# Kernel optimization log

Measured on AMD Instinct MI355X. Metric: run time of the kernel, lower is better.

The kernel has to match this reference:

```python
import jax, jax.numpy as jnp
import numpy as np

NEG_SLOPE = 0.2  # LeakyReLU slope from the module


def setup_inputs() -> dict:
    key = jax.random.key(0)
    k1, k2, k3, k4 = jax.random.split(key, 4)
    B, N, C, H, D = 8, 1024, 256, 4, 64
    x = jax.random.normal(k1, (B, N, C), dtype=jnp.float32)
    adj = (jax.random.uniform(k2, (B, N, N)) < 0.05).astype(jnp.float32)
    # nn.Linear weight, stored as (in, out) for x @ W
    W = jax.random.normal(k3, (C, H * D), dtype=jnp.float32) / np.sqrt(C)
    a = jax.random.normal(k4, (1, H, 2 * D), dtype=jnp.float32) * 0.1
    return {"x": x, "adj": adj, "W": W, "a": a}


def reference(x, adj, W, a):
    # x: (B,N,C), adj: (B,N,N), W: (C,H*D), a: (1,H,2D)
    B, N, _ = x.shape
    H = a.shape[1]
    D = a.shape[2] // 2
    Wx = (x @ W).reshape(B, N, H, D)  # (B,N,H,D)
    # (cat([Wx_i, Wx_j]) * a).sum(-1) decomposes into two rank-1 terms:
    a_i, a_j = a[0, :, :D], a[0, :, D:]
    e_i = jnp.einsum('bnhd,hd->bnh', Wx, a_i)  # contribution of target node i
    e_j = jnp.einsum('bjhd,hd->bjh', Wx, a_j)  # contribution of source node j
    e = e_i[:, :, None, :] + e_j[:, None, :, :]  # (B,N,N,H)
    e = jnp.where(e > 0, e, NEG_SLOPE * e)  # LeakyReLU(0.2)
    # add self-loops, mask non-edges with -inf
    adj_self = adj + jnp.eye(N, dtype=adj.dtype)[None]
    mask = (adj_self == 0)[..., None]  # (B,N,N,1)
    e = jnp.where(mask, -jnp.inf, e)
    alpha = jax.nn.softmax(e, axis=2)  # softmax over neighbors j
    # dropout is identity in eval mode
    # torch: einsum('bnjh,bnjhd', alpha, Wx_j) with Wx_j broadcast over n
    out = jnp.einsum('bnjh,bjhd->bnhd', alpha, Wx)
    return out.reshape(B, N, H * D)
```

## Files before the change

### kernel.cpp

```cpp
#include <hip/hip_runtime.h>

#define Nn 1024
#define Cc 256
#define Hh 4
#define Dd 64
#define HD 256
#define LOG2E 1.4426950408889634f
#define WSTRIDE 264

typedef unsigned short u16;
typedef unsigned int u32;
typedef unsigned long long u64;
typedef unsigned char u8;
typedef __bf16 bf16x2 __attribute__((ext_vector_type(2)));
typedef __bf16 bf16x8 __attribute__((ext_vector_type(8)));
typedef float f32x4 __attribute__((ext_vector_type(4)));
typedef u16 u16x8 __attribute__((ext_vector_type(8)));
typedef u32 u32x4 __attribute__((ext_vector_type(4)));

__device__ __forceinline__ float bf2f(u16 v) {
    return __builtin_bit_cast(float, (u32)v << 16);
}
__device__ __forceinline__ u16 f2bf(float f) {
    u32 u = __builtin_bit_cast(u32, f);
    return (u16)((u + 0x7fffu + ((u >> 16) & 1u)) >> 16);
}
__device__ __forceinline__ u32 pk_bf16(float a, float b) {
#if __has_builtin(__builtin_amdgcn_cvt_pk_bf16_f32)
    bf16x2 v = __builtin_amdgcn_cvt_pk_bf16_f32(a, b);
    return __builtin_bit_cast(u32, v);
#else
    return (u32)f2bf(a) | ((u32)f2bf(b) << 16);
#endif
}
__device__ __forceinline__ float fast_exp2(float x) {
#if __has_builtin(__builtin_amdgcn_exp2f)
    return __builtin_amdgcn_exp2f(x);
#else
    float r; asm("v_exp_f32 %0, %1" : "=v"(r) : "v"(x)); return r;
#endif
}

__global__ __launch_bounds__(256) void k_fused(const float* __restrict__ adj,
        u8* __restrict__ bm, const float* __restrict__ x,
        const float* __restrict__ W, const float* __restrict__ a,
        u16* __restrict__ WxTt, float* __restrict__ ei, float* __restrict__ ej) {
    __shared__ u16 ldsw[Dd * WSTRIDE];

    if (blockIdx.x >= 512) {
        int idx = (blockIdx.x - 512) * 256 + threadIdx.x;
        int bn = idx >> 7;
        int byteidx = idx & 127;
        int n = bn & 1023;
        const float* p = adj + ((size_t)bn << 10) + (byteidx << 3);
        float4 v0 = *reinterpret_cast<const float4*>(p);
        float4 v1 = *reinterpret_cast<const float4*>(p + 4);
        u32 bits = 0;
        bits |= (__builtin_bit_cast(u32, v0.x) != 0u) ? 1u : 0u;
        bits |= (__builtin_bit_cast(u32, v0.y) != 0u) ? 2u : 0u;
        bits |= (__builtin_bit_cast(u32, v0.z) != 0u) ? 4u : 0u;
        bits |= (__builtin_bit_cast(u32, v0.w) != 0u) ? 8u : 0u;
        bits |= (__builtin_bit_cast(u32, v1.x) != 0u) ? 16u : 0u;
        bits |= (__builtin_bit_cast(u32, v1.y) != 0u) ? 32u : 0u;
        bits |= (__builtin_bit_cast(u32, v1.z) != 0u) ? 64u : 0u;
        bits |= (__builtin_bit_cast(u32, v1.w) != 0u) ? 128u : 0u;
        if ((n >> 3) == byteidx) bits |= 1u << (n & 7);
        bm[idx] = (u8)bits;
        return;
    }

    int h = blockIdx.x & 3;
    int group = blockIdx.x >> 2;
    int tid = threadIdx.x;

    {
        const float* wrow = W + tid * HD + h * 64;
        #pragma unroll
        for (int c = 0; c < 64; c += 4) {
            float4 wv = *reinterpret_cast<const float4*>(wrow + c);
            u32 p01 = pk_bf16(wv.x, wv.y);
            u32 p23 = pk_bf16(wv.z, wv.w);
            ldsw[(c + 0) * WSTRIDE + tid] = (u16)p01;
            ldsw[(c + 1) * WSTRIDE + tid] = (u16)(p01 >> 16);
            ldsw[(c + 2) * WSTRIDE + tid] = (u16)p23;
            ldsw[(c + 3) * WSTRIDE + tid] = (u16)(p23 >> 16);
        }
    }
    __syncthreads();

    int w = tid >> 6, lane = tid & 63;
    int row_tile = group * 4 + w;
    int m0 = row_tile * 16;
    int b = m0 >> 10;
    int nloc0 = m0 & 1023;
    int c15 = lane & 15;
    int quad = lane >> 4;

    f32x4 acc[4] = {};
    const float* xrow = x + (size_t)(m0 + c15) * Cc + quad * 8;
    #pragma unroll
    for (int k0 = 0; k0 < Cc; k0 += 32) {
        float4 xv0 = *reinterpret_cast<const float4*>(xrow + k0);
        float4 xv1 = *reinterpret_cast<const float4*>(xrow + k0 + 4);
        u32 h0 = pk_bf16(xv0.x, xv0.y);
        u32 h1 = pk_bf16(xv0.z, xv0.w);
        u32 h2 = pk_bf16(xv1.x, xv1.y);
        u32 h3 = pk_bf16(xv1.z, xv1.w);
        u32 l0 = pk_bf16(xv0.x - __builtin_bit_cast(float, h0 << 16),
                         xv0.y - __builtin_bit_cast(float, h0 & 0xffff0000u));
        u32 l1 = pk_bf16(xv0.z - __builtin_bit_cast(float, h1 << 16),
                         xv0.w - __builtin_bit_cast(float, h1 & 0xffff0000u));
        u32 l2 = pk_bf16(xv1.x - __builtin_bit_cast(float, h2 << 16),
                         xv1.y - __builtin_bit_cast(float, h2 & 0xffff0000u));
        u32 l3 = pk_bf16(xv1.z - __builtin_bit_cast(float, h3 << 16),
                         xv1.w - __builtin_bit_cast(float, h3 & 0xffff0000u));
        u32x4 hp = {h0, h1, h2, h3};
        u32x4 lp = {l0, l1, l2, l3};
        bf16x8 ah = __builtin_bit_cast(bf16x8, hp);
        bf16x8 al = __builtin_bit_cast(bf16x8, lp);
        const u16* ldsk = ldsw + k0 + quad * 8;
        #pragma unroll
        for (int t = 0; t < 4; ++t) {
            bf16x8 bh = *reinterpret_cast<const bf16x8*>(ldsk + (t * 16 + c15) * WSTRIDE);
            acc[t] = __builtin_amdgcn_mfma_f32_16x16x32_bf16(ah, bh, acc[t], 0, 0, 0);
            acc[t] = __builtin_amdgcn_mfma_f32_16x16x32_bf16(al, bh, acc[t], 0, 0, 0);
        }
    }
    int bh = b * Hh + h;
    int n_base = nloc0 + quad * 4;
    int chunk = nloc0 >> 5;
    int jq = ((n_base >> 3) & 3);
    int ii = n_base & 7;
    size_t tb = (size_t)bh * 65536 + chunk * 2048 + jq * 128 + c15 * 8 + ii;
    #pragma unroll
    for (int t = 0; t < 4; ++t) {
        uint2 pk2;
        pk2.x = pk_bf16(acc[t][0], acc[t][1]);
        pk2.y = pk_bf16(acc[t][2], acc[t][3]);
        *reinterpret_cast<uint2*>(WxTt + tb + t * 512) = pk2;
    }
    float ai[4], aj[4];
    #pragma unroll
    for (int t = 0; t < 4; ++t) {
        ai[t] = a[h * 2 * Dd + t * 16 + c15];
        aj[t] = a[h * 2 * Dd + Dd + t * 16 + c15];
    }
    #pragma unroll
    for (int r = 0; r < 4; ++r) {
        float si = acc[0][r] * ai[0] + acc[1][r] * ai[1] + acc[2][r] * ai[2] + acc[3][r] * ai[3];
        float sj = acc[0][r] * aj[0] + acc[1][r] * aj[1] + acc[2][r] * aj[2] + acc[3][r] * aj[3];
        #pragma unroll
        for (int off = 1; off < 16; off <<= 1) {
            si += __shfl_xor(si, off);
            sj += __shfl_xor(sj, off);
        }
        if (c15 == 0) {
            int n = nloc0 + quad * 4 + r;
            ei[(size_t)bh * Nn + n] = si * LOG2E;
            ej[(size_t)bh * Nn + n] = sj * LOG2E;
        }
    }
}

__global__ __launch_bounds__(256) void k_attn(const u8* __restrict__ bm,
        const u16* __restrict__ WxTt, const float* __restrict__ eis,
        const float* __restrict__ ejs, float* __restrict__ out) {
    int widx = threadIdx.x >> 6;
    int lane = threadIdx.x & 63;
    int bh = blockIdx.x >> 5;
    int tile = blockIdx.x & 31;
    int b = bh >> 2, h = bh & 3;
    int n0 = tile * 32;
    int col = lane & 15;
    int quad = lane >> 4;

    int r0 = n0 + col, r1 = n0 + 16 + col;
    float ei0 = eis[(size_t)bh * Nn + r0];
    float ei1 = eis[(size_t)bh * Nn + r1];
    const u8* mb0 = bm + ((size_t)(b * Nn + r0)) * 128;
    const u8* mb1 = bm + ((size_t)(b * Nn + r1)) * 128;
    const float* ejrow = ejs + (size_t)bh * Nn + quad * 8;
    const u16* wxplane = WxTt + (size_t)bh * 65536 + lane * 8;

    u16 ov = (col == 0) ? (u16)0x3f80 : (u16)0;
    u16x8 onesu = {ov, ov, ov, ov, ov, ov, ov, ov};
    bf16x8 onesf = __builtin_bit_cast(bf16x8, onesu);

    f32x4 acc0[4] = {}, acc1[4] = {};
    f32x4 accl0 = {}, accl1 = {};
    int jbase = widx * 256;
    #pragma unroll 2
    for (int s = 0; s < 8; ++s) {
        int j0 = jbase + s * 32;
        u32 mw0 = *reinterpret_cast<const u32*>(mb0 + (j0 >> 3));
        u32 mw1 = *reinterpret_cast<const u32*>(mb1 + (j0 >> 3));
        u32 q0 = (mw0 >> (quad * 8)) & 0xffu;
        u32 q1 = (mw1 >> (quad * 8)) & 0xffu;
        float4 eA = *reinterpret_cast<const float4*>(ejrow + j0);
        float4 eB = *reinterpret_cast<const float4*>(ejrow + j0 + 4);
        float ejv[8] = {eA.x, eA.y, eA.z, eA.w, eB.x, eB.y, eB.z, eB.w};
        u32 p0[4], p1[4];
        #pragma unroll
        for (int pi = 0; pi < 4; ++pi) {
            float e_lo = ejv[2 * pi], e_hi = ejv[2 * pi + 1];
            float sa = ei0 + e_lo, sb = ei0 + e_hi;
            sa = fmaxf(sa, 0.2f * sa); sb = fmaxf(sb, 0.2f * sb);
            u32 m0 = (((q0 >> (2 * pi)) & 1u) ? 0xffffu : 0u)
                   | (((q0 >> (2 * pi + 1)) & 1u) ? 0xffff0000u : 0u);
            p0[pi] = pk_bf16(fast_exp2(sa), fast_exp2(sb)) & m0;
            float sc = ei1 + e_lo, sd = ei1 + e_hi;
            sc = fmaxf(sc, 0.2f * sc); sd = fmaxf(sd, 0.2f * sd);
            u32 m1 = (((q1 >> (2 * pi)) & 1u) ? 0xffffu : 0u)
                   | (((q1 >> (2 * pi + 1)) & 1u) ? 0xffff0000u : 0u);
            p1[pi] = pk_bf16(fast_exp2(sc), fast_exp2(sd)) & m1;
        }
        u32x4 pv0 = {p0[0], p0[1], p0[2], p0[3]};
        u32x4 pv1 = {p1[0], p1[1], p1[2], p1[3]};
        bf16x8 a0 = __builtin_bit_cast(bf16x8, pv0);
        bf16x8 a1 = __builtin_bit_cast(bf16x8, pv1);
        const u16* bbase = wxplane + (j0 >> 5) * 2048;
        #pragma unroll
        for (int t = 0; t < 4; ++t) {
            bf16x8 bfr = *reinterpret_cast<const bf16x8*>(bbase + t * 512);
            acc0[t] = __builtin_amdgcn_mfma_f32_16x16x32_bf16(a0, bfr, acc0[t], 0, 0, 0);
            acc1[t] = __builtin_amdgcn_mfma_f32_16x16x32_bf16(a1, bfr, acc1[t], 0, 0, 0);
        }
        accl0 = __builtin_amdgcn_mfma_f32_16x16x32_bf16(a0, onesf, accl0, 0, 0, 0);
        accl1 = __builtin_amdgcn_mfma_f32_16x16x32_bf16(a1, onesf, accl1, 0, 0, 0);
    }

    __shared__ f32x4 lacc[4][8][64];
    __shared__ float lsums[4][2][16];
    #pragma unroll
    for (int t = 0; t < 4; ++t) {
        lacc[widx][t][lane] = acc0[t];
        lacc[widx][4 + t][lane] = acc1[t];
    }
    if (col == 0) {
        #pragma unroll
        for (int r = 0; r < 4; ++r) {
            lsums[widx][0][quad * 4 + r] = accl0[r];
            lsums[widx][1][quad * 4 + r] = accl1[r];
        }
    }
    __syncthreads();
    #pragma unroll
    for (int pp = 0; pp < 2; ++pp) {
        int p = widx * 2 + pp;
        int f = p >> 2, t = p & 3;
        f32x4 v = lacc[0][p][lane];
        v += lacc[1][p][lane];
        v += lacc[2][p][lane];
        v += lacc[3][p][lane];
        #pragma unroll
        for (int r = 0; r < 4; ++r) {
            int rloc = quad * 4 + r;
            float lv = lsums[0][f][rloc] + lsums[1][f][rloc]
                     + lsums[2][f][rloc] + lsums[3][f][rloc];
            int nr = n0 + f * 16 + rloc;
            out[(size_t)(b * Nn + nr) * HD + h * Dd + t * 16 + col] = v[r] * (1.0f / lv);
        }
    }
}

extern "C" void kernel_launch(void* const* d_in, const int* in_sizes, int n_in,
                              void* d_out, int out_size, void* d_ws, size_t ws_size,
                              hipStream_t stream) {
    const float* x   = (const float*)d_in[0];
    const float* adj = (const float*)d_in[1];
    const float* W   = (const float*)d_in[2];
    const float* a   = (const float*)d_in[3];
    float* out = (float*)d_out;

    char* ws = (char*)d_ws;
    u16*   WxTt = (u16*)(ws);
    float* ei   = (float*)(ws + (4u << 20));
    float* ej   = (float*)(ws + (4u << 20) + (128u << 10));
    u8*    bm   = (u8*)(ws + (4u << 20) + (256u << 10));

    k_fused<<<4608, 256, 0, stream>>>(adj, bm, x, W, a, WxTt, ei, ej);
    k_attn<<<1024, 256, 0, stream>>>(bm, WxTt, ei, ej, out);
}
```

Measured before the change: 111.8 us.

## Fuse adjacency bitmask packing into attention kernel and split work across heads

After: 139.2 us. 24.5% more time.

```diff
diff --git a/kernel.cpp b/kernel.cpp
--- a/kernel.cpp
+++ b/kernel.cpp
@@ -10,7 +10,6 @@
 
 typedef unsigned short u16;
 typedef unsigned int u32;
-typedef unsigned long long u64;
 typedef unsigned char u8;
 typedef __bf16 bf16x2 __attribute__((ext_vector_type(2)));
 typedef __bf16 bf16x8 __attribute__((ext_vector_type(8)));
@@ -41,33 +40,10 @@
 #endif
 }
 
-__global__ __launch_bounds__(256) void k_fused(const float* __restrict__ adj,
-        u8* __restrict__ bm, const float* __restrict__ x,
+__global__ __launch_bounds__(256) void k_gemm(const float* __restrict__ x,
         const float* __restrict__ W, const float* __restrict__ a,
         u16* __restrict__ WxTt, float* __restrict__ ei, float* __restrict__ ej) {
     __shared__ u16 ldsw[Dd * WSTRIDE];
-
-    if (blockIdx.x >= 512) {
-        int idx = (blockIdx.x - 512) * 256 + threadIdx.x;
-        int bn = idx >> 7;
-        int byteidx = idx & 127;
-        int n = bn & 1023;
-        const float* p = adj + ((size_t)bn << 10) + (byteidx << 3);
-        float4 v0 = *reinterpret_cast<const float4*>(p);
-        float4 v1 = *reinterpret_cast<const float4*>(p + 4);
-        u32 bits = 0;
-        bits |= (__builtin_bit_cast(u32, v0.x) != 0u) ? 1u : 0u;
-        bits |= (__builtin_bit_cast(u32, v0.y) != 0u) ? 2u : 0u;
-        bits |= (__builtin_bit_cast(u32, v0.z) != 0u) ? 4u : 0u;
-        bits |= (__builtin_bit_cast(u32, v0.w) != 0u) ? 8u : 0u;
-        bits |= (__builtin_bit_cast(u32, v1.x) != 0u) ? 16u : 0u;
-        bits |= (__builtin_bit_cast(u32, v1.y) != 0u) ? 32u : 0u;
-        bits |= (__builtin_bit_cast(u32, v1.z) != 0u) ? 64u : 0u;
-        bits |= (__builtin_bit_cast(u32, v1.w) != 0u) ? 128u : 0u;
-        if ((n >> 3) == byteidx) bits |= 1u << (n & 7);
-        bm[idx] = (u8)bits;
-        return;
-    }
 
     int h = blockIdx.x & 3;
     int group = blockIdx.x >> 2;
@@ -162,103 +138,98 @@
     }
 }
 
-__global__ __launch_bounds__(256) void k_attn(const u8* __restrict__ bm,
+__global__ __launch_bounds__(512) void k_attn(const float* __restrict__ adj,
         const u16* __restrict__ WxTt, const float* __restrict__ eis,
         const float* __restrict__ ejs, float* __restrict__ out) {
-    int widx = threadIdx.x >> 6;
-    int lane = threadIdx.x & 63;
-    int bh = blockIdx.x >> 5;
+    __shared__ u32 maskLds[32][33];
+
+    int tid = threadIdx.x;
+    int b = blockIdx.x >> 5;
     int tile = blockIdx.x & 31;
-    int b = bh >> 2, h = bh & 3;
     int n0 = tile * 32;
+
+    {
+        int row = tid >> 4;
+        int w0 = (tid & 15) * 2;
+        int n = n0 + row;
+        const float* arow = adj + ((size_t)(b * Nn + n)) * Nn;
+        #pragma unroll
+        for (int wi = 0; wi < 2; ++wi) {
+            int w = w0 + wi;
+            const float* pw = arow + w * 32;
+            u32 bits = 0;
+            #pragma unroll
+            for (int g = 0; g < 8; ++g) {
+                float4 v = *reinterpret_cast<const float4*>(pw + g * 4);
+                bits |= (__builtin_bit_cast(u32, v.x) != 0u ? 1u : 0u) << (g * 4 + 0);
+                bits |= (__builtin_bit_cast(u32, v.y) != 0u ? 1u : 0u) << (g * 4 + 1);
+                bits |= (__builtin_bit_cast(u32, v.z) != 0u ? 1u : 0u) << (g * 4 + 2);
+                bits |= (__builtin_bit_cast(u32, v.w) != 0u ? 1u : 0u) << (g * 4 + 3);
+            }
+            if (w == (n >> 5)) bits |= 1u << (n & 31);
+            maskLds[row][w] = bits;
+        }
+    }
+    __syncthreads();
+
+    int wid = tid >> 6;
+    int lane = tid & 63;
+    int h = wid >> 1;
+    int rt = wid & 1;
+    int bh = b * Hh + h;
     int col = lane & 15;
     int quad = lane >> 4;
 
-    int r0 = n0 + col, r1 = n0 + 16 + col;
-    float ei0 = eis[(size_t)bh * Nn + r0];
-    float ei1 = eis[(size_t)bh * Nn + r1];
-    const u8* mb0 = bm + ((size_t)(b * Nn + r0)) * 128;
-    const u8* mb1 = bm + ((size_t)(b * Nn + r1)) * 128;
+    int arow_n = n0 + rt * 16 + col;
+    float ei_r = eis[(size_t)bh * Nn + arow_n];
     const float* ejrow = ejs + (size_t)bh * Nn + quad * 8;
     const u16* wxplane = WxTt + (size_t)bh * 65536 + lane * 8;
+    const u32* mrow = &maskLds[rt * 16 + col][0];
 
     u16 ov = (col == 0) ? (u16)0x3f80 : (u16)0;
     u16x8 onesu = {ov, ov, ov, ov, ov, ov, ov, ov};
     bf16x8 onesf = __builtin_bit_cast(bf16x8, onesu);
 
-    f32x4 acc0[4] = {}, acc1[4] = {};
-    f32x4 accl0 = {}, accl1 = {};
-    int jbase = widx * 256;
+    f32x4 acc[4] = {};
+    f32x4 accl = {};
     #pragma unroll 2
-    for (int s = 0; s < 8; ++s) {
-        int j0 = jbase + s * 32;
-        u32 mw0 = *reinterpret_cast<const u32*>(mb0 + (j0 >> 3));
-        u32 mw1 = *reinterpret_cast<const u32*>(mb1 + (j0 >> 3));
-        u32 q0 = (mw0 >> (quad * 8)) & 0xffu;
-        u32 q1 = (mw1 >> (quad * 8)) & 0xffu;
+    for (int s = 0; s < 32; ++s) {
+        int j0 = s * 32;
+        u32 mw = mrow[s];
+        u32 q0 = (mw >> (quad * 8)) & 0xffu;
         float4 eA = *reinterpret_cast<const float4*>(ejrow + j0);
         float4 eB = *reinterpret_cast<const float4*>(ejrow + j0 + 4);
         float ejv[8] = {eA.x, eA.y, eA.z, eA.w, eB.x, eB.y, eB.z, eB.w};
-        u32 p0[4], p1[4];
+        u32 p[4];
         #pragma unroll
         for (int pi = 0; pi < 4; ++pi) {
-            float e_lo = ejv[2 * pi], e_hi = ejv[2 * pi + 1];
-            float sa = ei0 + e_lo, sb = ei0 + e_hi;
+            float sa = ei_r + ejv[2 * pi];
+            float sb = ei_r + ejv[2 * pi + 1];
             sa = fmaxf(sa, 0.2f * sa); sb = fmaxf(sb, 0.2f * sb);
             u32 m0 = (((q0 >> (2 * pi)) & 1u) ? 0xffffu : 0u)
                    | (((q0 >> (2 * pi + 1)) & 1u) ? 0xffff0000u : 0u);
-            p0[pi] = pk_bf16(fast_exp2(sa), fast_exp2(sb)) & m0;
-            float sc = ei1 + e_lo, sd = ei1 + e_hi;
-            sc = fmaxf(sc, 0.2f * sc); sd = fmaxf(sd, 0.2f * sd);
-            u32 m1 = (((q1 >> (2 * pi)) & 1u) ? 0xffffu : 0u)
-                   | (((q1 >> (2 * pi + 1)) & 1u) ? 0xffff0000u : 0u);
-            p1[pi] = pk_bf16(fast_exp2(sc), fast_exp2(sd)) & m1;
-        }
-        u32x4 pv0 = {p0[0], p0[1], p0[2], p0[3]};
-        u32x4 pv1 = {p1[0], p1[1], p1[2], p1[3]};
-        bf16x8 a0 = __builtin_bit_cast(bf16x8, pv0);
-        bf16x8 a1 = __builtin_bit_cast(bf16x8, pv1);
-        const u16* bbase = wxplane + (j0 >> 5) * 2048;
+            p[pi] = pk_bf16(fast_exp2(sa), fast_exp2(sb)) & m0;
+        }
+        u32x4 pv = {p[0], p[1], p[2], p[3]};
+        bf16x8 afr = __builtin_bit_cast(bf16x8, pv);
+        const u16* bbase = wxplane + s * 2048;
         #pragma unroll
         for (int t = 0; t < 4; ++t) {
             bf16x8 bfr = *reinterpret_cast<const bf16x8*>(bbase + t * 512);
-            acc0[t] = __builtin_amdgcn_mfma_f32_16x16x32_bf16(a0, bfr, acc0[t], 0, 0, 0);
-            acc1[t] = __builtin_amdgcn_mfma_f32_16x16x32_bf16(a1, bfr, acc1[t], 0, 0, 0);
-        }
-        accl0 = __builtin_amdgcn_mfma_f32_16x16x32_bf16(a0, onesf, accl0, 0, 0, 0);
-        accl1 = __builtin_amdgcn_mfma_f32_16x16x32_bf16(a1, onesf, accl1, 0, 0, 0);
-    }
-
-    __shared__ f32x4 lacc[4][8][64];
-    __shared__ float lsums[4][2][16];
-    #pragma unroll
-    for (int t = 0; t < 4; ++t) {
-        lacc[widx][t][lane] = acc0[t];
-        lacc[widx][4 + t][lane] = acc1[t];
-    }
-    if (col == 0) {
-        #pragma unroll
-        for (int r = 0; r < 4; ++r) {
-            lsums[widx][0][quad * 4 + r] = accl0[r];
-            lsums[widx][1][quad * 4 + r] = accl1[r];
-        }
-    }
-    __syncthreads();
-    #pragma unroll
-    for (int pp = 0; pp < 2; ++pp) {
-        int p = widx * 2 + pp;
-        int f = p >> 2, t = p & 3;
-        f32x4 v = lacc[0][p][lane];
-        v += lacc[1][p][lane];
-        v += lacc[2][p][lane];
-        v += lacc[3][p][lane];
-        #pragma unroll
-        for (int r = 0; r < 4; ++r) {
-            int rloc = quad * 4 + r;
-            float lv = lsums[0][f][rloc] + lsums[1][f][rloc]
-                     + lsums[2][f][rloc] + lsums[3][f][rloc];
-            int nr = n0 + f * 16 + rloc;
-            out[(size_t)(b * Nn + nr) * HD + h * Dd + t * 16 + col] = v[r] * (1.0f / lv);
+            acc[t] = __builtin_amdgcn_mfma_f32_16x16x32_bf16(afr, bfr, acc[t], 0, 0, 0);
+        }
+        accl = __builtin_amdgcn_mfma_f32_16x16x32_bf16(afr, onesf, accl, 0, 0, 0);
+    }
+
+    #pragma unroll
+    for (int r = 0; r < 4; ++r) {
+        float lv = __shfl(accl[r], quad << 4);
+        float inv = 1.0f / lv;
+        int nr = n0 + rt * 16 + quad * 4 + r;
+        size_t obase = ((size_t)(b * Nn + nr)) * HD + h * Dd;
+        #pragma unroll
+        for (int t = 0; t < 4; ++t) {
+            out[obase + t * 16 + col] = acc[t][r] * inv;
         }
     }
 }
@@ -276,8 +247,7 @@
     u16*   WxTt = (u16*)(ws);
     float* ei   = (float*)(ws + (4u << 20));
     float* ej   = (float*)(ws + (4u << 20) + (128u << 10));
-    u8*    bm   = (u8*)(ws + (4u << 20) + (256u << 10));
-
-    k_fused<<<4608, 256, 0, stream>>>(adj, bm, x, W, a, WxTt, ei, ej);
-    k_attn<<<1024, 256, 0, stream>>>(bm, WxTt, ei, ej, out);
-}
+
+    k_gemm<<<512, 256, 0, stream>>>(x, W, a, WxTt, ei, ej);
+    k_attn<<<256, 512, 0, stream>>>(adj, WxTt, ei, ej, out);
+}
```
